# Kernel tuning notes

Measured on AMD Instinct MI355X. Metric: run time of the kernel, lower is better.

## Reference

```python
import jax, jax.numpy as jnp
import numpy as np

LN_EPS = 1e-5

def _layer_norm(x, gamma, beta):
    m = jnp.mean(x, axis=-1, keepdims=True)
    v = jnp.mean((x - m) ** 2, axis=-1, keepdims=True)
    return (x - m) / jnp.sqrt(v + LN_EPS) * gamma + beta

def setup_inputs() -> dict:
    key = jax.random.key(0)
    k1, k2, k3 = jax.random.split(key, 3)
    N, E, D = 8192, 4096, 128
    node_embeddings = jax.random.normal(k1, (N, D), dtype=jnp.float32)
    target_matrix = jax.random.normal(k2, (N, N), dtype=jnp.float32)
    hypergraph_matrix = jax.random.randint(k3, (N, E), 0, 2, dtype=jnp.int32)
    ln_gamma = jnp.ones((D,), dtype=jnp.float32)
    ln_beta = jnp.zeros((D,), dtype=jnp.float32)
    return {
        "node_embeddings": node_embeddings,
        "target_matrix": target_matrix,
        "ln_gamma": ln_gamma,
        "ln_beta": ln_beta,
        "hypergraph_matrix": hypergraph_matrix,
        "num_layers": 3,
    }

def reference(node_embeddings, target_matrix, ln_gamma, ln_beta, hypergraph_matrix, num_layers):
    x = node_embeddings  # [N, D]
    for _ in range(num_layers):
        t = jnp.matmul(target_matrix, x)        # [N, D]
        x = jnp.matmul(target_matrix.T, t)      # [N, D]
        x = _layer_norm(x, ln_gamma, ln_beta)
        # dropout is identity in eval mode
    # per-hyperedge masked mean over nodes, vectorized as a dense GEMV-style reduce
    h = (hypergraph_matrix > 0).astype(x.dtype)            # [N, E]
    counts = jnp.sum(h, axis=0)                            # [E]
    sums = jnp.einsum('ne,nd->ed', h, x)                   # [E, D]
    means = sums / counts[:, None]                         # [E, D]
    return jnp.max(means, axis=0)                          # [D]
```

## Files before the change

### kernel.cpp

```cpp
#include <hip/hip_runtime.h>
#include <cstdint>
#include <cstddef>

typedef __attribute__((ext_vector_type(8))) short short8;
typedef __attribute__((ext_vector_type(4))) short short4v;
typedef __attribute__((ext_vector_type(4))) float float4v;
typedef __attribute__((ext_vector_type(4))) int int4v;
typedef unsigned short ushort_t;

__device__ __forceinline__ ushort_t f2bf(float f) {
  unsigned u = __builtin_bit_cast(unsigned, f);
  u = (u + 0x7FFFu + ((u >> 16) & 1u)) >> 16;
  return (ushort_t)u;
}
__device__ __forceinline__ float bf2f(ushort_t h) {
  unsigned u = ((unsigned)h) << 16;
  return __builtin_bit_cast(float, u);
}

__device__ __forceinline__ void gld_lds16(const void* g, void* l) {
  __builtin_amdgcn_global_load_lds(
      (const __attribute__((address_space(1))) void*)g,
      (__attribute__((address_space(3))) void*)l, 16, 0, 0);
}

__global__ __launch_bounds__(256, 2) void gemm_tn(
    const ushort_t* __restrict__ A, const ushort_t* __restrict__ B,
    float* __restrict__ P, int M, int N, int K, int kslice) {
  __shared__ ushort_t As[128 * 64];
  __shared__ ushort_t Bs[128 * 64];
  const int tid = threadIdx.x;
  const int lane = tid & 63;
  const int wave = tid >> 6;
  const int wm = (wave & 1) * 64;
  const int wn = (wave >> 1) * 64;
  const int m0 = blockIdx.x * 128;
  const int n0 = blockIdx.y * 128;
  const int k0 = blockIdx.z * kslice;
  float* __restrict__ Pc = P + (size_t)blockIdx.z * M * N;

  float4v acc[4][4] = {};

  for (int kt = 0; kt < kslice; kt += 64) {
    const ushort_t* Ag = A + (size_t)m0 * K + (k0 + kt);
    const ushort_t* Bg = B + (size_t)n0 * K + (k0 + kt);
#pragma unroll
    for (int i = 0; i < 4; i++) {
      int f = i * 4096 + tid * 16;
      int r = f >> 7;
      int cb = f & 127;
      gld_lds16((const char*)(Ag + (size_t)r * K) + cb, (char*)As + f);
      gld_lds16((const char*)(Bg + (size_t)r * K) + cb, (char*)Bs + f);
    }
    __syncthreads();
#pragma unroll
    for (int ks = 0; ks < 64; ks += 32) {
      short8 af[4], bfr[4];
      const int kr = ks + (lane >> 4) * 8;
      const int l15 = lane & 15;
#pragma unroll
      for (int im = 0; im < 4; im++)
        af[im] = *(const short8*)&As[(wm + im * 16 + l15) * 64 + kr];
#pragma unroll
      for (int in = 0; in < 4; in++)
        bfr[in] = *(const short8*)&Bs[(wn + in * 16 + l15) * 64 + kr];
#pragma unroll
      for (int im = 0; im < 4; im++)
#pragma unroll
        for (int in = 0; in < 4; in++)
          acc[im][in] = __builtin_amdgcn_mfma_f32_16x16x32_bf16(
              af[im], bfr[in], acc[im][in], 0, 0, 0);
    }
    __syncthreads();
  }
  const int cn = lane & 15;
  const int cr = (lane >> 4) * 4;
#pragma unroll
  for (int im = 0; im < 4; im++)
#pragma unroll
    for (int in = 0; in < 4; in++)
#pragma unroll
      for (int r = 0; r < 4; r++) {
        int m = wm + im * 16 + cr + r;
        int n = wn + in * 16 + cn;
        Pc[(size_t)(m0 + m) * N + (n0 + n)] = acc[im][in][r];
      }
}

__global__ __launch_bounds__(256) void dualcast_f32_k(
    const float* __restrict__ src, ushort_t* __restrict__ dstN,
    ushort_t* __restrict__ dstT, int R, int C) {
  __shared__ float tile[64][65];
  const int r0 = blockIdx.x * 64, c0 = blockIdx.y * 64;
  const int tr = threadIdx.x >> 2, cs = (threadIdx.x & 3) * 16;
  const float* s = src + (size_t)(r0 + tr) * C + c0 + cs;
  float v[16];
#pragma unroll
  for (int j = 0; j < 16; j += 4) {
    float4v t4 = *(const float4v*)(s + j);
    v[j] = t4.x; v[j + 1] = t4.y; v[j + 2] = t4.z; v[j + 3] = t4.w;
  }
#pragma unroll
  for (int j = 0; j < 16; j++) tile[tr][cs + j] = v[j];
  if (dstN) {
    short8 o[2];
#pragma unroll
    for (int j = 0; j < 16; j++) ((ushort_t*)o)[j] = f2bf(v[j]);
    ushort_t* d = dstN + (size_t)(r0 + tr) * C + c0 + cs;
    *(short8*)d = o[0];
    *(short8*)(d + 8) = o[1];
  }
  __syncthreads();
  const int tc = threadIdx.x >> 2, rs = (threadIdx.x & 3) * 16;
  short8 o[2];
#pragma unroll
  for (int j = 0; j < 16; j++) ((ushort_t*)o)[j] = f2bf(tile[rs + j][tc]);
  ushort_t* d = dstT + (size_t)(c0 + tc) * R + r0 + rs;
  *(short8*)d = o[0];
  *(short8*)(d + 8) = o[1];
}

__global__ __launch_bounds__(256) void tcast_i32_k(
    const int* __restrict__ src, ushort_t* __restrict__ dstT, int R, int C) {
  __shared__ float tile[64][65];
  const int r0 = blockIdx.x * 64, c0 = blockIdx.y * 64;
  const int tr = threadIdx.x >> 2, cs = (threadIdx.x & 3) * 16;
  const int* s = src + (size_t)(r0 + tr) * C + c0 + cs;
#pragma unroll
  for (int j = 0; j < 16; j += 4) {
    int4v t4 = *(const int4v*)(s + j);
    tile[tr][cs + j] = t4.x > 0 ? 1.f : 0.f;
    tile[tr][cs + j + 1] = t4.y > 0 ? 1.f : 0.f;
    tile[tr][cs + j + 2] = t4.z > 0 ? 1.f : 0.f;
    tile[tr][cs + j + 3] = t4.w > 0 ? 1.f : 0.f;
  }
  __syncthreads();
  const int tc = threadIdx.x >> 2, rs = (threadIdx.x & 3) * 16;
  short8 o[2];
#pragma unroll
  for (int j = 0; j < 16; j++) ((ushort_t*)o)[j] = f2bf(tile[rs + j][tc]);
  ushort_t* d = dstT + (size_t)(c0 + tc) * R + r0 + rs;
  *(short8*)d = o[0];
  *(short8*)(d + 8) = o[1];
}

__global__ __launch_bounds__(256) void transpose_bf16_k(
    const ushort_t* __restrict__ src, ushort_t* __restrict__ dst, int R, int C) {
  __shared__ ushort_t tile[64][66];
  const int r0 = blockIdx.x * 64, c0 = blockIdx.y * 64;
  const int tr = threadIdx.x >> 2, cs = (threadIdx.x & 3) * 16;
  const ushort_t* s = src + (size_t)(r0 + tr) * C + c0 + cs;
  short8 v0 = *(const short8*)s, v1 = *(const short8*)(s + 8);
#pragma unroll
  for (int j = 0; j < 8; j++) {
    tile[tr][cs + j] = ((ushort_t*)&v0)[j];
    tile[tr][cs + 8 + j] = ((ushort_t*)&v1)[j];
  }
  __syncthreads();
  const int tc = threadIdx.x >> 2, rs = (threadIdx.x & 3) * 16;
  short8 o[2];
#pragma unroll
  for (int j = 0; j < 16; j++) ((ushort_t*)o)[j] = tile[rs + j][tc];
  ushort_t* d = dst + (size_t)(c0 + tc) * R + r0 + rs;
  *(short8*)d = o[0];
  *(short8*)(d + 8) = o[1];
}

__global__ __launch_bounds__(256) void counts_k(
    const ushort_t* __restrict__ hT, float* __restrict__ counts, int Nn) {
  const int e = blockIdx.x * 4 + (threadIdx.x >> 6);
  const int lane = threadIdx.x & 63;
  const ushort_t* row = hT + (size_t)e * Nn;
  float s = 0.f;
  for (int i = 0; i < Nn / 512; i++) {
    short8 v = *(const short8*)&row[i * 512 + lane * 8];
#pragma unroll
    for (int j = 0; j < 8; j++) s += bf2f(((ushort_t*)&v)[j]);
  }
#pragma unroll
  for (int off = 32; off > 0; off >>= 1) s += __shfl_down(s, off);
  if (lane == 0) counts[e] = s;
}

__global__ __launch_bounds__(256) void reduce_bf16_k(
    const float* __restrict__ P, ushort_t* __restrict__ out, int MN, int S) {
  const int i = (blockIdx.x * 256 + threadIdx.x) * 4;
  if (i >= MN) return;
  float4v s = {0.f, 0.f, 0.f, 0.f};
  for (int sp = 0; sp < S; sp++) s += *(const float4v*)&P[(size_t)sp * MN + i];
  short4v o;
#pragma unroll
  for (int j = 0; j < 4; j++) ((ushort_t*)&o)[j] = f2bf(s[j]);
  *(short4v*)&out[i] = o;
}

__global__ __launch_bounds__(256) void reduce_ln_k(
    const float* __restrict__ P, const float* __restrict__ gamma,
    const float* __restrict__ beta, float* __restrict__ xo, int MN) {
  const int m = blockIdx.x * 4 + (threadIdx.x >> 6);
  const int lane = threadIdx.x & 63;
  const float* base = P + (size_t)m * 128 + lane;
  float v0 = 0.f, v1 = 0.f;
  for (int sp = 0; sp < 8; sp++) {
    v0 += base[(size_t)sp * MN];
    v1 += base[(size_t)sp * MN + 64];
  }
  float s = v0 + v1, sq = v0 * v0 + v1 * v1;
#pragma unroll
  for (int off = 32; off > 0; off >>= 1) {
    s += __shfl_down(s, off);
    sq += __shfl_down(sq, off);
  }
  s = __shfl(s, 0);
  sq = __shfl(sq, 0);
  const float mean = s * (1.f / 128.f);
  const float var = sq * (1.f / 128.f) - mean * mean;
  const float inv = rsqrtf(var + 1e-5f);
  xo[(size_t)m * 128 + lane] = (v0 - mean) * inv * gamma[lane] + beta[lane];
  xo[(size_t)m * 128 + lane + 64] =
      (v1 - mean) * inv * gamma[lane + 64] + beta[lane + 64];
}

__global__ __launch_bounds__(128) void mm1_k(
    const float* __restrict__ P, const float* __restrict__ counts,
    float* __restrict__ pm, int E, int D) {
  const int d = threadIdx.x;
  float vmax = -3.4e38f;
  const int e0 = blockIdx.x * 128;
  for (int e = e0; e < e0 + 128; e++) {
    float s = 0.f;
    for (int sp = 0; sp < 8; sp++)
      s += P[(size_t)sp * E * D + (size_t)e * D + d];
    vmax = fmaxf(vmax, s / counts[e]);
  }
  pm[blockIdx.x * 128 + d] = vmax;
}

__global__ __launch_bounds__(128) void mm2_k(
    const float* __restrict__ pm, float* __restrict__ out, int B) {
  const int d = threadIdx.x;
  float v = -3.4e38f;
  for (int b = 0; b < B; b++) v = fmaxf(v, pm[b * 128 + d]);
  out[d] = v;
}

extern "C" void kernel_launch(void* const* d_in, const int* in_sizes, int n_in,
                              void* d_out, int out_size, void* d_ws,
                              size_t ws_size, hipStream_t stream) {
  const float* x0 = (const float*)d_in[0];
  const float* T = (const float*)d_in[1];
  const float* gamma = (const float*)d_in[2];
  const float* beta = (const float*)d_in[3];
  const int* h = (const int*)d_in[4];
  float* out = (float*)d_out;

  const int N = 8192, E = 4096, D = 128, K = 8192, S = 8;

  char* ws = (char*)d_ws;
  size_t off = 0;
  auto alloc = [&](size_t bytes) {
    char* p = ws + off;
    off += (bytes + 255) & ~(size_t)255;
    return p;
  };
  ushort_t* Tb = (ushort_t*)alloc((size_t)N * N * 2);
  ushort_t* Tt = (ushort_t*)alloc((size_t)N * N * 2);
  ushort_t* hT = (ushort_t*)alloc((size_t)E * N * 2);
  ushort_t* xT = (ushort_t*)alloc((size_t)D * N * 2);
  ushort_t* tT = (ushort_t*)alloc((size_t)D * N * 2);
  ushort_t* trm = (ushort_t*)alloc((size_t)N * D * 2);
  float* xlnf = (float*)alloc((size_t)N * D * 4);
  float* P = (float*)alloc((size_t)S * N * D * 4);
  float* counts = (float*)alloc((size_t)E * 4);
  float* pm = (float*)alloc((size_t)32 * D * 4);
  (void)ws_size;

  dualcast_f32_k<<<dim3(N / 64, N / 64), 256, 0, stream>>>(T, Tb, Tt, N, N);
  dualcast_f32_k<<<dim3(N / 64, D / 64), 256, 0, stream>>>(x0, nullptr, xT, N, D);
  tcast_i32_k<<<dim3(N / 64, E / 64), 256, 0, stream>>>(h, hT, N, E);
  counts_k<<<E / 4, 256, 0, stream>>>(hT, counts, N);

  for (int layer = 0; layer < 3; layer++) {
    gemm_tn<<<dim3(N / 128, D / 128, S), 256, 0, stream>>>(Tb, xT, P, N, D, K,
                                                           K / S);
    reduce_bf16_k<<<(N * D / 4 + 255) / 256, 256, 0, stream>>>(P, trm, N * D, S);
    transpose_bf16_k<<<dim3(N / 64, D / 64), 256, 0, stream>>>(trm, tT, N, D);
    gemm_tn<<<dim3(N / 128, D / 128, S), 256, 0, stream>>>(Tt, tT, P, N, D, K,
                                                           K / S);
    reduce_ln_k<<<N / 4, 256, 0, stream>>>(P, gamma, beta, xlnf, N * D);
    dualcast_f32_k<<<dim3(N / 64, D / 64), 256, 0, stream>>>(xlnf, nullptr, xT,
                                                             N, D);
  }
  gemm_tn<<<dim3(E / 128, D / 128, S), 256, 0, stream>>>(hT, xT, P, E, D, K,
                                                         K / S);
  mm1_k<<<E / 128, 128, 0, stream>>>(P, counts, pm, E, D);
  mm2_k<<<1, 128, 0, stream>>>(pm, out, 32);
}
```

Baseline: 966.6 us.

## Use atomic split-K accumulation with transposed GEMM output and fused LN-cast kernels

The split-K GEMMs now accumulate directly into one fp32 buffer with atomic adds instead of writing per-slice partials. Operands are swapped so each GEMM produces the D×N transposed layout that the next GEMM consumes. This removes the separate reduce and transpose kernels, and LayerNorm, bf16 cast and buffer re-zeroing are fused into single passes. It also doubles the K-split count, makes the cast kernels stage bf16 in LDS and use nontemporal loads, and adds an upfront memset of the accumulator. In exchange it adds atomic contention, a non-deterministic summation order, and strided column access in the LN kernel.

```diff
diff --git a/kernel.cpp b/kernel.cpp
--- a/kernel.cpp
+++ b/kernel.cpp
@@ -37,7 +37,6 @@
   const int m0 = blockIdx.x * 128;
   const int n0 = blockIdx.y * 128;
   const int k0 = blockIdx.z * kslice;
-  float* __restrict__ Pc = P + (size_t)blockIdx.z * M * N;
 
   float4v acc[4][4] = {};
 
@@ -83,87 +82,67 @@
       for (int r = 0; r < 4; r++) {
         int m = wm + im * 16 + cr + r;
         int n = wn + in * 16 + cn;
-        Pc[(size_t)(m0 + m) * N + (n0 + n)] = acc[im][in][r];
+        unsafeAtomicAdd(&P[(size_t)(m0 + m) * N + (n0 + n)], acc[im][in][r]);
       }
 }
 
 __global__ __launch_bounds__(256) void dualcast_f32_k(
     const float* __restrict__ src, ushort_t* __restrict__ dstN,
     ushort_t* __restrict__ dstT, int R, int C) {
-  __shared__ float tile[64][65];
+  __shared__ ushort_t tile[64][72];
   const int r0 = blockIdx.x * 64, c0 = blockIdx.y * 64;
   const int tr = threadIdx.x >> 2, cs = (threadIdx.x & 3) * 16;
   const float* s = src + (size_t)(r0 + tr) * C + c0 + cs;
-  float v[16];
+  ushort_t v[16];
 #pragma unroll
   for (int j = 0; j < 16; j += 4) {
-    float4v t4 = *(const float4v*)(s + j);
-    v[j] = t4.x; v[j + 1] = t4.y; v[j + 2] = t4.z; v[j + 3] = t4.w;
-  }
-#pragma unroll
-  for (int j = 0; j < 16; j++) tile[tr][cs + j] = v[j];
+    float4v t4 = __builtin_nontemporal_load((const float4v*)(s + j));
+    v[j] = f2bf(t4.x); v[j + 1] = f2bf(t4.y);
+    v[j + 2] = f2bf(t4.z); v[j + 3] = f2bf(t4.w);
+  }
   if (dstN) {
-    short8 o[2];
-#pragma unroll
-    for (int j = 0; j < 16; j++) ((ushort_t*)o)[j] = f2bf(v[j]);
     ushort_t* d = dstN + (size_t)(r0 + tr) * C + c0 + cs;
-    *(short8*)d = o[0];
-    *(short8*)(d + 8) = o[1];
-  }
+    *(short8*)d = *(const short8*)&v[0];
+    *(short8*)(d + 8) = *(const short8*)&v[8];
+  }
+  *(short8*)&tile[tr][cs] = *(const short8*)&v[0];
+  *(short8*)&tile[tr][cs + 8] = *(const short8*)&v[8];
   __syncthreads();
   const int tc = threadIdx.x >> 2, rs = (threadIdx.x & 3) * 16;
-  short8 o[2];
-#pragma unroll
-  for (int j = 0; j < 16; j++) ((ushort_t*)o)[j] = f2bf(tile[rs + j][tc]);
+  ushort_t o[16];
+#pragma unroll
+  for (int j = 0; j < 16; j++) o[j] = tile[rs + j][tc];
   ushort_t* d = dstT + (size_t)(c0 + tc) * R + r0 + rs;
-  *(short8*)d = o[0];
-  *(short8*)(d + 8) = o[1];
+  *(short8*)d = *(const short8*)&o[0];
+  *(short8*)(d + 8) = *(const short8*)&o[8];
 }
 
 __global__ __launch_bounds__(256) void tcast_i32_k(
     const int* __restrict__ src, ushort_t* __restrict__ dstT, int R, int C) {
-  __shared__ float tile[64][65];
+  __shared__ ushort_t tile[64][72];
   const int r0 = blockIdx.x * 64, c0 = blockIdx.y * 64;
   const int tr = threadIdx.x >> 2, cs = (threadIdx.x & 3) * 16;
   const int* s = src + (size_t)(r0 + tr) * C + c0 + cs;
+  const ushort_t one = 0x3F80, zero = 0;
+  ushort_t v[16];
 #pragma unroll
   for (int j = 0; j < 16; j += 4) {
-    int4v t4 = *(const int4v*)(s + j);
-    tile[tr][cs + j] = t4.x > 0 ? 1.f : 0.f;
-    tile[tr][cs + j + 1] = t4.y > 0 ? 1.f : 0.f;
-    tile[tr][cs + j + 2] = t4.z > 0 ? 1.f : 0.f;
-    tile[tr][cs + j + 3] = t4.w > 0 ? 1.f : 0.f;
-  }
+    int4v t4 = __builtin_nontemporal_load((const int4v*)(s + j));
+    v[j] = t4.x > 0 ? one : zero;
+    v[j + 1] = t4.y > 0 ? one : zero;
+    v[j + 2] = t4.z > 0 ? one : zero;
+    v[j + 3] = t4.w > 0 ? one : zero;
+  }
+  *(short8*)&tile[tr][cs] = *(const short8*)&v[0];
+  *(short8*)&tile[tr][cs + 8] = *(const short8*)&v[8];
   __syncthreads();
   const int tc = threadIdx.x >> 2, rs = (threadIdx.x & 3) * 16;
-  short8 o[2];
-#pragma unroll
-  for (int j = 0; j < 16; j++) ((ushort_t*)o)[j] = f2bf(tile[rs + j][tc]);
+  ushort_t o[16];
+#pragma unroll
+  for (int j = 0; j < 16; j++) o[j] = tile[rs + j][tc];
   ushort_t* d = dstT + (size_t)(c0 + tc) * R + r0 + rs;
-  *(short8*)d = o[0];
-  *(short8*)(d + 8) = o[1];
-}
-
-__global__ __launch_bounds__(256) void transpose_bf16_k(
-    const ushort_t* __restrict__ src, ushort_t* __restrict__ dst, int R, int C) {
-  __shared__ ushort_t tile[64][66];
-  const int r0 = blockIdx.x * 64, c0 = blockIdx.y * 64;
-  const int tr = threadIdx.x >> 2, cs = (threadIdx.x & 3) * 16;
-  const ushort_t* s = src + (size_t)(r0 + tr) * C + c0 + cs;
-  short8 v0 = *(const short8*)s, v1 = *(const short8*)(s + 8);
-#pragma unroll
-  for (int j = 0; j < 8; j++) {
-    tile[tr][cs + j] = ((ushort_t*)&v0)[j];
-    tile[tr][cs + 8 + j] = ((ushort_t*)&v1)[j];
-  }
-  __syncthreads();
-  const int tc = threadIdx.x >> 2, rs = (threadIdx.x & 3) * 16;
-  short8 o[2];
-#pragma unroll
-  for (int j = 0; j < 16; j++) ((ushort_t*)o)[j] = tile[rs + j][tc];
-  ushort_t* d = dst + (size_t)(c0 + tc) * R + r0 + rs;
-  *(short8*)d = o[0];
-  *(short8*)(d + 8) = o[1];
+  *(short8*)d = *(const short8*)&o[0];
+  *(short8*)(d + 8) = *(const short8*)&o[8];
 }
 
 __global__ __launch_bounds__(256) void counts_k(
@@ -182,57 +161,56 @@
   if (lane == 0) counts[e] = s;
 }
 
-__global__ __launch_bounds__(256) void reduce_bf16_k(
-    const float* __restrict__ P, ushort_t* __restrict__ out, int MN, int S) {
-  const int i = (blockIdx.x * 256 + threadIdx.x) * 4;
-  if (i >= MN) return;
-  float4v s = {0.f, 0.f, 0.f, 0.f};
-  for (int sp = 0; sp < S; sp++) s += *(const float4v*)&P[(size_t)sp * MN + i];
-  short4v o;
-#pragma unroll
-  for (int j = 0; j < 4; j++) ((ushort_t*)&o)[j] = f2bf(s[j]);
-  *(short4v*)&out[i] = o;
-}
-
-__global__ __launch_bounds__(256) void reduce_ln_k(
-    const float* __restrict__ P, const float* __restrict__ gamma,
-    const float* __restrict__ beta, float* __restrict__ xo, int MN) {
-  const int m = blockIdx.x * 4 + (threadIdx.x >> 6);
-  const int lane = threadIdx.x & 63;
-  const float* base = P + (size_t)m * 128 + lane;
-  float v0 = 0.f, v1 = 0.f;
-  for (int sp = 0; sp < 8; sp++) {
-    v0 += base[(size_t)sp * MN];
-    v1 += base[(size_t)sp * MN + 64];
-  }
-  float s = v0 + v1, sq = v0 * v0 + v1 * v1;
-#pragma unroll
-  for (int off = 32; off > 0; off >>= 1) {
-    s += __shfl_down(s, off);
-    sq += __shfl_down(sq, off);
-  }
-  s = __shfl(s, 0);
-  sq = __shfl(sq, 0);
-  const float mean = s * (1.f / 128.f);
-  const float var = sq * (1.f / 128.f) - mean * mean;
+__global__ __launch_bounds__(256) void cast_zero_k(
+    float* __restrict__ P, ushort_t* __restrict__ out) {
+  const int i = (blockIdx.x * 256 + threadIdx.x) * 8;
+  float4v a = *(const float4v*)&P[i];
+  float4v b = *(const float4v*)&P[i + 4];
+  ushort_t o[8];
+  o[0] = f2bf(a.x); o[1] = f2bf(a.y); o[2] = f2bf(a.z); o[3] = f2bf(a.w);
+  o[4] = f2bf(b.x); o[5] = f2bf(b.y); o[6] = f2bf(b.z); o[7] = f2bf(b.w);
+  *(short8*)&out[i] = *(const short8*)o;
+  float4v z = {0.f, 0.f, 0.f, 0.f};
+  *(float4v*)&P[i] = z;
+  *(float4v*)&P[i + 4] = z;
+}
+
+__global__ __launch_bounds__(256) void ln_cast_zero_k(
+    float* __restrict__ P, const float* __restrict__ gamma,
+    const float* __restrict__ beta, ushort_t* __restrict__ xT, int Ncols) {
+  __shared__ float ssum[4][64], ssq[4][64];
+  const int m = blockIdx.x * 64 + (threadIdx.x & 63);
+  const int q = threadIdx.x >> 6;
+  float s = 0.f, sq = 0.f;
+  for (int d = q * 32; d < q * 32 + 32; d++) {
+    float v = P[(size_t)d * Ncols + m];
+    s += v; sq += v * v;
+  }
+  ssum[q][threadIdx.x & 63] = s;
+  ssq[q][threadIdx.x & 63] = sq;
+  __syncthreads();
+  const int c = threadIdx.x & 63;
+  float S = ssum[0][c] + ssum[1][c] + ssum[2][c] + ssum[3][c];
+  float SQ = ssq[0][c] + ssq[1][c] + ssq[2][c] + ssq[3][c];
+  const float mean = S * (1.f / 128.f);
+  const float var = SQ * (1.f / 128.f) - mean * mean;
   const float inv = rsqrtf(var + 1e-5f);
-  xo[(size_t)m * 128 + lane] = (v0 - mean) * inv * gamma[lane] + beta[lane];
-  xo[(size_t)m * 128 + lane + 64] =
-      (v1 - mean) * inv * gamma[lane + 64] + beta[lane + 64];
+  for (int d = q * 32; d < q * 32 + 32; d++) {
+    size_t idx = (size_t)d * Ncols + m;
+    float v = P[idx];
+    xT[idx] = f2bf((v - mean) * inv * gamma[d] + beta[d]);
+    P[idx] = 0.f;
+  }
 }
 
 __global__ __launch_bounds__(128) void mm1_k(
     const float* __restrict__ P, const float* __restrict__ counts,
-    float* __restrict__ pm, int E, int D) {
+    float* __restrict__ pm) {
   const int d = threadIdx.x;
   float vmax = -3.4e38f;
   const int e0 = blockIdx.x * 128;
-  for (int e = e0; e < e0 + 128; e++) {
-    float s = 0.f;
-    for (int sp = 0; sp < 8; sp++)
-      s += P[(size_t)sp * E * D + (size_t)e * D + d];
-    vmax = fmaxf(vmax, s / counts[e]);
-  }
+  for (int e = e0; e < e0 + 128; e++)
+    vmax = fmaxf(vmax, P[(size_t)e * 128 + d] / counts[e]);
   pm[blockIdx.x * 128 + d] = vmax;
 }
 
@@ -254,7 +232,7 @@
   const int* h = (const int*)d_in[4];
   float* out = (float*)d_out;
 
-  const int N = 8192, E = 4096, D = 128, K = 8192, S = 8;
+  const int N = 8192, E = 4096, D = 128, K = 8192, S = 16;
 
   char* ws = (char*)d_ws;
   size_t off = 0;
@@ -268,12 +246,12 @@
   ushort_t* hT = (ushort_t*)alloc((size_t)E * N * 2);
   ushort_t* xT = (ushort_t*)alloc((size_t)D * N * 2);
   ushort_t* tT = (ushort_t*)alloc((size_t)D * N * 2);
-  ushort_t* trm = (ushort_t*)alloc((size_t)N * D * 2);
-  float* xlnf = (float*)alloc((size_t)N * D * 4);
-  float* P = (float*)alloc((size_t)S * N * D * 4);
+  float* P = (float*)alloc((size_t)D * N * 4);
   float* counts = (float*)alloc((size_t)E * 4);
   float* pm = (float*)alloc((size_t)32 * D * 4);
   (void)ws_size;
+
+  hipMemsetAsync(P, 0, (size_t)D * N * 4 + 256  + (size_t)E * 4, stream);
 
   dualcast_f32_k<<<dim3(N / 64, N / 64), 256, 0, stream>>>(T, Tb, Tt, N, N);
   dualcast_f32_k<<<dim3(N / 64, D / 64), 256, 0, stream>>>(x0, nullptr, xT, N, D);
@@ -281,18 +259,12 @@
   counts_k<<<E / 4, 256, 0, stream>>>(hT, counts, N);
 
   for (int layer = 0; layer < 3; layer++) {
-    gemm_tn<<<dim3(N / 128, D / 128, S), 256, 0, stream>>>(Tb, xT, P, N, D, K,
-                                                           K / S);
-    reduce_bf16_k<<<(N * D / 4 + 255) / 256, 256, 0, stream>>>(P, trm, N * D, S);
-    transpose_bf16_k<<<dim3(N / 64, D / 64), 256, 0, stream>>>(trm, tT, N, D);
-    gemm_tn<<<dim3(N / 128, D / 128, S), 256, 0, stream>>>(Tt, tT, P, N, D, K,
-                                                           K / S);
-    reduce_ln_k<<<N / 4, 256, 0, stream>>>(P, gamma, beta, xlnf, N * D);
-    dualcast_f32_k<<<dim3(N / 64, D / 64), 256, 0, stream>>>(xlnf, nullptr, xT,
-                                                             N, D);
-  }
-  gemm_tn<<<dim3(E / 128, D / 128, S), 256, 0, stream>>>(hT, xT, P, E, D, K,
-                                                         K / S);
-  mm1_k<<<E / 128, 128, 0, stream>>>(P, counts, pm, E, D);
-  mm2_k<<<1, 128, 0, stream>>>(pm, out, 32);
-}
+    gemm_tn<<<dim3(1, N / 128, S), 256, 0, stream>>>(xT, Tb, P, D, N, K, K / S);
+    cast_zero_k<<<D * N / (256 * 8), 256, 0, stream>>>(P, tT);
+    gemm_tn<<<dim3(1, N / 128, S), 256, 0, stream>>>(tT, Tt, P, D, N, K, K / S);
+    ln_cast_zero_k<<<N / 64, 256, 0, stream>>>(P, gamma, beta, xT, N);
+  }
+  gemm_tn<<<dim3(E / 128, 1, S), 256, 0, stream>>>(hT, xT, P, E, D, K, K / S);
+  mm1_k<<<E / 128, 128, 0, stream>>>(P, counts, pm);
+  mm2_k<<<1, 128, 0, stream>>>(pm, out, E / 128);
+}
```

Result: slower. 1.093 ms (+13.1%).
